# Kernel optimization log

Measured on AMD Instinct MI355X. Metric: run time of the kernel, lower is better.

Reference implementation:

```python
import jax, jax.numpy as jnp
import numpy as np

D_IN, D_H1, D_H2, D_OUT = 24, 64, 128, 64

def setup_inputs() -> dict:
    key = jax.random.key(0)
    ks = jax.random.split(key, 7)
    B, L = 256, 2048
    input_data = jax.random.normal(ks[0], (B, L, D_IN), dtype=jnp.float32)
    s = lambda fan_in: 1.0 / np.sqrt(fan_in)
    W1 = jax.random.uniform(ks[1], (D_IN, D_H1), minval=-s(D_IN), maxval=s(D_IN), dtype=jnp.float32)
    b1 = jax.random.uniform(ks[2], (D_H1,), minval=-s(D_IN), maxval=s(D_IN), dtype=jnp.float32)
    W2 = jax.random.uniform(ks[3], (D_H1, D_H2), minval=-s(D_H1), maxval=s(D_H1), dtype=jnp.float32)
    b2 = jax.random.uniform(ks[4], (D_H2,), minval=-s(D_H1), maxval=s(D_H1), dtype=jnp.float32)
    W3 = jax.random.uniform(ks[5], (D_H2, D_OUT), minval=-s(D_H2), maxval=s(D_H2), dtype=jnp.float32)
    b3 = jax.random.uniform(ks[6], (D_OUT,), minval=-s(D_H2), maxval=s(D_H2), dtype=jnp.float32)
    return {"input_data": input_data, "W1": W1, "b1": b1, "W2": W2, "b2": b2, "W3": W3, "b3": b3, "batch_size": 256}

def reference(input_data, W1, b1, W2, b2, W3, b3, batch_size):
    # Vectorized equivalent of the per-(batch,line) MLP loop:
    # three Linear+ReLU layers applied to every [24]-dim vector.
    h = jax.nn.relu(jnp.einsum('bli,ij->blj', input_data, W1) + b1)
    h = jax.nn.relu(jnp.einsum('bli,ij->blj', h, W2) + b2)
    out = jax.nn.relu(jnp.einsum('bli,ij->blj', h, W3) + b3)  # [B, L, 64]
    return out
```

## Files before the change

kernel.cpp:

```cpp
#include <hip/hip_runtime.h>

typedef float f32x4 __attribute__((ext_vector_type(4)));
typedef short s16x8 __attribute__((ext_vector_type(8)));
typedef unsigned int u32;

#define DIN 24
#define DH1 64
#define DH2 128
#define DOUT 64
#define S1 72
#define S2 136

static __device__ __forceinline__ unsigned short f2bf(float f) {
    u32 u = __builtin_bit_cast(u32, f);
    u += 0x7FFFu + ((u >> 16) & 1u);
    return (unsigned short)(u >> 16);
}

static __device__ __forceinline__ u32 cvtpk(float lo, float hi) {
    u32 r;
    asm("v_cvt_pk_bf16_f32 %0, %1, %2" : "=v"(r) : "v"(lo), "v"(hi));
    return r;
}

__global__ __launch_bounds__(256, 2) void linenet_mfma_t(
    const float* __restrict__ in,
    const float* __restrict__ W1, const float* __restrict__ b1,
    const float* __restrict__ W2, const float* __restrict__ b2,
    const float* __restrict__ W3, const float* __restrict__ b3,
    float* __restrict__ out, int M)
{
    __shared__ __align__(16) unsigned short h1lds[4][1152];
    __shared__ __align__(16) unsigned short h2lds[4][2176];

    const int tid  = threadIdx.x;
    const int wave = tid >> 6, lane = tid & 63;
    const int gl = lane >> 4, cl = lane & 15;

    s16x8 w1tf[4];
    #pragma unroll
    for (int nt = 0; nt < 4; ++nt)
        #pragma unroll
        for (int j = 0; j < 8; ++j) {
            const int k = 8 * gl + j;
            unsigned short v = 0;
            if (k < DIN)       v = f2bf(W1[k * DH1 + nt * 16 + cl]);
            else if (k == DIN) v = f2bf(b1[nt * 16 + cl]);
            w1tf[nt][j] = (short)v;
        }
    s16x8 w2tf[8][2];
    #pragma unroll
    for (int mt = 0; mt < 8; ++mt)
        #pragma unroll
        for (int ks = 0; ks < 2; ++ks)
            #pragma unroll
            for (int j = 0; j < 8; ++j)
                w2tf[mt][ks][j] =
                    (short)f2bf(W2[(32 * ks + 8 * gl + j) * DH2 + mt * 16 + cl]);
    s16x8 w3tf[4][4];
    #pragma unroll
    for (int nt = 0; nt < 4; ++nt)
        #pragma unroll
        for (int ks = 0; ks < 4; ++ks)
            #pragma unroll
            for (int j = 0; j < 8; ++j)
                w3tf[nt][ks][j] =
                    (short)f2bf(W3[(32 * ks + 8 * gl + j) * DOUT + nt * 16 + cl]);

    f32x4 b2v4[8], b3v4[4];
    #pragma unroll
    for (int mt = 0; mt < 8; ++mt) b2v4[mt] = *(const f32x4*)&b2[16 * mt + 4 * gl];
    #pragma unroll
    for (int nt = 0; nt < 4; ++nt) b3v4[nt] = *(const f32x4*)&b3[16 * nt + 4 * gl];

    unsigned short* const h1p = &h1lds[wave][0];
    unsigned short* const h2p = &h2lds[wave][0];

    const int NT = M / 16;
    const int nw = (int)gridDim.x * 4;
    int t = (int)blockIdx.x * 4 + wave;
    if (t >= NT) return;

    const int goff = (gl < 3) ? 8 * gl : 0;
    const int loff = cl * DIN + goff;

    f32x4 pf0, pf1;
    {
        const float* p = in + (size_t)t * (16 * DIN) + loff;
        pf0 = *(const f32x4*)p;
        pf1 = *(const f32x4*)(p + 4);
    }

    const f32x4 zac = {0.f, 0.f, 0.f, 0.f};

    while (t < NT) {
        u32 a1w[4];
        a1w[0] = cvtpk(pf0[0], pf0[1]);
        a1w[1] = cvtpk(pf0[2], pf0[3]);
        a1w[2] = cvtpk(pf1[0], pf1[1]);
        a1w[3] = cvtpk(pf1[2], pf1[3]);
        if (gl == 3) a1w[0] = 0x00003F80u;
        s16x8 a1;
        #pragma unroll
        for (int p = 0; p < 4; ++p) {
            a1[2 * p]     = (short)(a1w[p] & 0xFFFFu);
            a1[2 * p + 1] = (short)(a1w[p] >> 16);
        }

        const int tn = t + nw;
        {
            const int tc = (tn < NT) ? tn : t;
            const float* p = in + (size_t)tc * (16 * DIN) + loff;
            pf0 = *(const f32x4*)p;
            pf1 = *(const f32x4*)(p + 4);
        }

        f32x4 acc1[4];
        #pragma unroll
        for (int nt = 0; nt < 4; ++nt)
            acc1[nt] = __builtin_amdgcn_mfma_f32_16x16x32_bf16(w1tf[nt], a1, zac, 0, 0, 0);

        #pragma unroll
        for (int nt = 0; nt < 4; ++nt) {
            const float v0 = fmaxf(acc1[nt][0], 0.f), v1 = fmaxf(acc1[nt][1], 0.f);
            const float v2 = fmaxf(acc1[nt][2], 0.f), v3 = fmaxf(acc1[nt][3], 0.f);
            u32* w = (u32*)&h1p[cl * S1 + 16 * nt + 4 * gl];
            w[0] = cvtpk(v0, v1);
            w[1] = cvtpk(v2, v3);
        }

        s16x8 bh1[2];
        bh1[0] = *(const s16x8*)&h1p[cl * S1 + 0  + 8 * gl];
        bh1[1] = *(const s16x8*)&h1p[cl * S1 + 32 + 8 * gl];
        f32x4 acc2[8];
        #pragma unroll
        for (int mt = 0; mt < 8; ++mt)
            acc2[mt] = __builtin_amdgcn_mfma_f32_16x16x32_bf16(w2tf[mt][0], bh1[0], zac, 0, 0, 0);
        #pragma unroll
        for (int mt = 0; mt < 8; ++mt)
            acc2[mt] = __builtin_amdgcn_mfma_f32_16x16x32_bf16(w2tf[mt][1], bh1[1], acc2[mt], 0, 0, 0);

        #pragma unroll
        for (int mt = 0; mt < 8; ++mt) {
            const f32x4 s = acc2[mt] + b2v4[mt];
            const float v0 = fmaxf(s[0], 0.f), v1 = fmaxf(s[1], 0.f);
            const float v2 = fmaxf(s[2], 0.f), v3 = fmaxf(s[3], 0.f);
            u32* w = (u32*)&h2p[cl * S2 + 16 * mt + 4 * gl];
            w[0] = cvtpk(v0, v1);
            w[1] = cvtpk(v2, v3);
        }

        f32x4 acc3[4];
        #pragma unroll
        for (int ks = 0; ks < 4; ++ks) {
            const s16x8 bh2 = *(const s16x8*)&h2p[cl * S2 + 32 * ks + 8 * gl];
            #pragma unroll
            for (int nt = 0; nt < 4; ++nt)
                acc3[nt] = __builtin_amdgcn_mfma_f32_16x16x32_bf16(
                    w3tf[nt][ks], bh2, (ks == 0) ? zac : acc3[nt], 0, 0, 0);
        }

        float* const ob = out + (size_t)t * (16 * DOUT) + (size_t)cl * DOUT;
        #pragma unroll
        for (int nt = 0; nt < 4; ++nt) {
            const f32x4 s = acc3[nt] + b3v4[nt];
            f32x4 v;
            v[0] = fmaxf(s[0], 0.f); v[1] = fmaxf(s[1], 0.f);
            v[2] = fmaxf(s[2], 0.f); v[3] = fmaxf(s[3], 0.f);
            *(f32x4*)&ob[16 * nt + 4 * gl] = v;
        }

        t = tn;
    }
}

extern "C" void kernel_launch(void* const* d_in, const int* in_sizes, int n_in,
                              void* d_out, int out_size, void* d_ws, size_t ws_size,
                              hipStream_t stream)
{
    const float* in = (const float*)d_in[0];
    const float* W1 = (const float*)d_in[1];
    const float* b1 = (const float*)d_in[2];
    const float* W2 = (const float*)d_in[3];
    const float* b2 = (const float*)d_in[4];
    const float* W3 = (const float*)d_in[5];
    const float* b3 = (const float*)d_in[6];
    float* out = (float*)d_out;
    const int M = in_sizes[0] / DIN;

    dim3 grid(512), block(256);
    hipLaunchKernelGGL(linenet_mfma_t, grid, block, 0, stream,
                       in, W1, b1, W2, b2, W3, b3, out, M);
}
```

Baseline: 43.85 us.

## Move W1/W3 fragments to LDS, fold biases into accumulators, raise occupancy

W1 and W3 MFMA fragments move from per-thread registers into shared LDS, loaded once per block, to free VGPRs. Launch bounds go from 2 to 3 blocks per CU and the grid from 512 to 768. Biases b2/b3 are stored packed as bf16 and used as the initial MFMA accumulator instead of added afterwards. Layer 2 is split into halves to shorten live ranges, and outputs use nontemporal stores. The cost is extra LDS reads per tile, and biases are now rounded to bf16.

```diff
diff --git a/kernel.cpp b/kernel.cpp
--- a/kernel.cpp
+++ b/kernel.cpp
@@ -3,6 +3,8 @@
 typedef float f32x4 __attribute__((ext_vector_type(4)));
 typedef short s16x8 __attribute__((ext_vector_type(8)));
 typedef unsigned int u32;
+typedef unsigned int u32x4 __attribute__((ext_vector_type(4)));
+typedef unsigned short u16;
 
 #define DIN 24
 #define DH1 64
@@ -11,10 +13,10 @@
 #define S1 72
 #define S2 136
 
-static __device__ __forceinline__ unsigned short f2bf(float f) {
+static __device__ __forceinline__ u16 f2bf(float f) {
     u32 u = __builtin_bit_cast(u32, f);
     u += 0x7FFFu + ((u >> 16) & 1u);
-    return (unsigned short)(u >> 16);
+    return (u16)(u >> 16);
 }
 
 static __device__ __forceinline__ u32 cvtpk(float lo, float hi) {
@@ -23,31 +25,53 @@
     return r;
 }
 
-__global__ __launch_bounds__(256, 2) void linenet_mfma_t(
+static __device__ __forceinline__ float bflo(u32 pk) {
+    return __builtin_bit_cast(float, pk << 16);
+}
+static __device__ __forceinline__ float bfhi(u32 pk) {
+    return __builtin_bit_cast(float, pk & 0xFFFF0000u);
+}
+
+__global__ __launch_bounds__(256, 3) void linenet_mfma3(
     const float* __restrict__ in,
     const float* __restrict__ W1, const float* __restrict__ b1,
     const float* __restrict__ W2, const float* __restrict__ b2,
     const float* __restrict__ W3, const float* __restrict__ b3,
     float* __restrict__ out, int M)
 {
-    __shared__ __align__(16) unsigned short h1lds[4][1152];
-    __shared__ __align__(16) unsigned short h2lds[4][2176];
+    __shared__ __align__(16) u16 w1lds[4 * 64 * 8];
+    __shared__ __align__(16) u16 w3lds[16 * 64 * 8];
+    __shared__ __align__(16) u16 h1lds[4][16 * S1];
+    __shared__ __align__(16) u16 h2lds[4][16 * S2];
 
     const int tid  = threadIdx.x;
     const int wave = tid >> 6, lane = tid & 63;
     const int gl = lane >> 4, cl = lane & 15;
 
-    s16x8 w1tf[4];
-    #pragma unroll
-    for (int nt = 0; nt < 4; ++nt)
+    {
+        const int nt = tid >> 6, ln = tid & 63;
+        const int g = ln >> 4, c = ln & 15;
+        s16x8 v;
         #pragma unroll
         for (int j = 0; j < 8; ++j) {
-            const int k = 8 * gl + j;
-            unsigned short v = 0;
-            if (k < DIN)       v = f2bf(W1[k * DH1 + nt * 16 + cl]);
-            else if (k == DIN) v = f2bf(b1[nt * 16 + cl]);
-            w1tf[nt][j] = (short)v;
-        }
+            const int k = 8 * g + j;
+            u16 x = 0;
+            if (k < DIN)       x = f2bf(W1[k * DH1 + nt * 16 + c]);
+            else if (k == DIN) x = f2bf(b1[nt * 16 + c]);
+            v[j] = (short)x;
+        }
+        *(s16x8*)&w1lds[tid * 8] = v;
+    }
+    for (int it = tid; it < 16 * 64; it += 256) {
+        const int f = it >> 6, ln = it & 63;
+        const int ks = f >> 2, nt = f & 3, g = ln >> 4, c = ln & 15;
+        s16x8 v;
+        #pragma unroll
+        for (int j = 0; j < 8; ++j)
+            v[j] = (short)f2bf(W3[(32 * ks + 8 * g + j) * DOUT + nt * 16 + c]);
+        *(s16x8*)&w3lds[it * 8] = v;
+    }
+
     s16x8 w2tf[8][2];
     #pragma unroll
     for (int mt = 0; mt < 8; ++mt)
@@ -57,24 +81,25 @@
             for (int j = 0; j < 8; ++j)
                 w2tf[mt][ks][j] =
                     (short)f2bf(W2[(32 * ks + 8 * gl + j) * DH2 + mt * 16 + cl]);
-    s16x8 w3tf[4][4];
+
+    u32 b2pk[8][2], b3pk[4][2];
+    #pragma unroll
+    for (int mt = 0; mt < 8; ++mt)
+        #pragma unroll
+        for (int p = 0; p < 2; ++p)
+            b2pk[mt][p] = (u32)f2bf(b2[16 * mt + 4 * gl + 2 * p]) |
+                          ((u32)f2bf(b2[16 * mt + 4 * gl + 2 * p + 1]) << 16);
     #pragma unroll
     for (int nt = 0; nt < 4; ++nt)
         #pragma unroll
-        for (int ks = 0; ks < 4; ++ks)
-            #pragma unroll
-            for (int j = 0; j < 8; ++j)
-                w3tf[nt][ks][j] =
-                    (short)f2bf(W3[(32 * ks + 8 * gl + j) * DOUT + nt * 16 + cl]);
-
-    f32x4 b2v4[8], b3v4[4];
-    #pragma unroll
-    for (int mt = 0; mt < 8; ++mt) b2v4[mt] = *(const f32x4*)&b2[16 * mt + 4 * gl];
-    #pragma unroll
-    for (int nt = 0; nt < 4; ++nt) b3v4[nt] = *(const f32x4*)&b3[16 * nt + 4 * gl];
-
-    unsigned short* const h1p = &h1lds[wave][0];
-    unsigned short* const h2p = &h2lds[wave][0];
+        for (int p = 0; p < 2; ++p)
+            b3pk[nt][p] = (u32)f2bf(b3[16 * nt + 4 * gl + 2 * p]) |
+                          ((u32)f2bf(b3[16 * nt + 4 * gl + 2 * p + 1]) << 16);
+
+    __syncthreads();
+
+    u16* const h1p = &h1lds[wave][0];
+    u16* const h2p = &h2lds[wave][0];
 
     const int NT = M / 16;
     const int nw = (int)gridDim.x * 4;
@@ -94,18 +119,13 @@
     const f32x4 zac = {0.f, 0.f, 0.f, 0.f};
 
     while (t < NT) {
-        u32 a1w[4];
-        a1w[0] = cvtpk(pf0[0], pf0[1]);
-        a1w[1] = cvtpk(pf0[2], pf0[3]);
-        a1w[2] = cvtpk(pf1[0], pf1[1]);
-        a1w[3] = cvtpk(pf1[2], pf1[3]);
-        if (gl == 3) a1w[0] = 0x00003F80u;
-        s16x8 a1;
-        #pragma unroll
-        for (int p = 0; p < 4; ++p) {
-            a1[2 * p]     = (short)(a1w[p] & 0xFFFFu);
-            a1[2 * p + 1] = (short)(a1w[p] >> 16);
-        }
+        u32x4 aw;
+        aw[0] = cvtpk(pf0[0], pf0[1]);
+        aw[1] = cvtpk(pf0[2], pf0[3]);
+        aw[2] = cvtpk(pf1[0], pf1[1]);
+        aw[3] = cvtpk(pf1[2], pf1[3]);
+        if (gl == 3) aw[0] = 0x00003F80u;
+        const s16x8 a1 = __builtin_bit_cast(s16x8, aw);
 
         const int tn = t + nw;
         {
@@ -117,9 +137,10 @@
 
         f32x4 acc1[4];
         #pragma unroll
-        for (int nt = 0; nt < 4; ++nt)
-            acc1[nt] = __builtin_amdgcn_mfma_f32_16x16x32_bf16(w1tf[nt], a1, zac, 0, 0, 0);
-
+        for (int nt = 0; nt < 4; ++nt) {
+            const s16x8 w1f = *(const s16x8*)&w1lds[(nt * 64 + lane) * 8];
+            acc1[nt] = __builtin_amdgcn_mfma_f32_16x16x32_bf16(w1f, a1, zac, 0, 0, 0);
+        }
         #pragma unroll
         for (int nt = 0; nt < 4; ++nt) {
             const float v0 = fmaxf(acc1[nt][0], 0.f), v1 = fmaxf(acc1[nt][1], 0.f);
@@ -132,42 +153,60 @@
         s16x8 bh1[2];
         bh1[0] = *(const s16x8*)&h1p[cl * S1 + 0  + 8 * gl];
         bh1[1] = *(const s16x8*)&h1p[cl * S1 + 32 + 8 * gl];
-        f32x4 acc2[8];
-        #pragma unroll
-        for (int mt = 0; mt < 8; ++mt)
-            acc2[mt] = __builtin_amdgcn_mfma_f32_16x16x32_bf16(w2tf[mt][0], bh1[0], zac, 0, 0, 0);
-        #pragma unroll
-        for (int mt = 0; mt < 8; ++mt)
-            acc2[mt] = __builtin_amdgcn_mfma_f32_16x16x32_bf16(w2tf[mt][1], bh1[1], acc2[mt], 0, 0, 0);
-
-        #pragma unroll
-        for (int mt = 0; mt < 8; ++mt) {
-            const f32x4 s = acc2[mt] + b2v4[mt];
-            const float v0 = fmaxf(s[0], 0.f), v1 = fmaxf(s[1], 0.f);
-            const float v2 = fmaxf(s[2], 0.f), v3 = fmaxf(s[3], 0.f);
-            u32* w = (u32*)&h2p[cl * S2 + 16 * mt + 4 * gl];
-            w[0] = cvtpk(v0, v1);
-            w[1] = cvtpk(v2, v3);
+
+        #pragma unroll
+        for (int half = 0; half < 2; ++half) {
+            f32x4 acc2[4];
+            #pragma unroll
+            for (int i = 0; i < 4; ++i) {
+                const int mt = 4 * half + i;
+                f32x4 c2;
+                c2[0] = bflo(b2pk[mt][0]); c2[1] = bfhi(b2pk[mt][0]);
+                c2[2] = bflo(b2pk[mt][1]); c2[3] = bfhi(b2pk[mt][1]);
+                acc2[i] = __builtin_amdgcn_mfma_f32_16x16x32_bf16(
+                    w2tf[mt][0], bh1[0], c2, 0, 0, 0);
+            }
+            #pragma unroll
+            for (int i = 0; i < 4; ++i) {
+                const int mt = 4 * half + i;
+                acc2[i] = __builtin_amdgcn_mfma_f32_16x16x32_bf16(
+                    w2tf[mt][1], bh1[1], acc2[i], 0, 0, 0);
+            }
+            #pragma unroll
+            for (int i = 0; i < 4; ++i) {
+                const int mt = 4 * half + i;
+                const float v0 = fmaxf(acc2[i][0], 0.f), v1 = fmaxf(acc2[i][1], 0.f);
+                const float v2 = fmaxf(acc2[i][2], 0.f), v3 = fmaxf(acc2[i][3], 0.f);
+                u32* w = (u32*)&h2p[cl * S2 + 16 * mt + 4 * gl];
+                w[0] = cvtpk(v0, v1);
+                w[1] = cvtpk(v2, v3);
+            }
         }
 
         f32x4 acc3[4];
+        #pragma unroll
+        for (int nt = 0; nt < 4; ++nt) {
+            acc3[nt][0] = bflo(b3pk[nt][0]); acc3[nt][1] = bfhi(b3pk[nt][0]);
+            acc3[nt][2] = bflo(b3pk[nt][1]); acc3[nt][3] = bfhi(b3pk[nt][1]);
+        }
         #pragma unroll
         for (int ks = 0; ks < 4; ++ks) {
             const s16x8 bh2 = *(const s16x8*)&h2p[cl * S2 + 32 * ks + 8 * gl];
             #pragma unroll
-            for (int nt = 0; nt < 4; ++nt)
+            for (int nt = 0; nt < 4; ++nt) {
+                const s16x8 wf = *(const s16x8*)&w3lds[((ks * 4 + nt) * 64 + lane) * 8];
                 acc3[nt] = __builtin_amdgcn_mfma_f32_16x16x32_bf16(
-                    w3tf[nt][ks], bh2, (ks == 0) ? zac : acc3[nt], 0, 0, 0);
+                    wf, bh2, acc3[nt], 0, 0, 0);
+            }
         }
 
         float* const ob = out + (size_t)t * (16 * DOUT) + (size_t)cl * DOUT;
         #pragma unroll
         for (int nt = 0; nt < 4; ++nt) {
-            const f32x4 s = acc3[nt] + b3v4[nt];
             f32x4 v;
-            v[0] = fmaxf(s[0], 0.f); v[1] = fmaxf(s[1], 0.f);
-            v[2] = fmaxf(s[2], 0.f); v[3] = fmaxf(s[3], 0.f);
-            *(f32x4*)&ob[16 * nt + 4 * gl] = v;
+            v[0] = fmaxf(acc3[nt][0], 0.f); v[1] = fmaxf(acc3[nt][1], 0.f);
+            v[2] = fmaxf(acc3[nt][2], 0.f); v[3] = fmaxf(acc3[nt][3], 0.f);
+            __builtin_nontemporal_store(v, (f32x4*)&ob[16 * nt + 4 * gl]);
         }
 
         t = tn;
@@ -188,7 +227,7 @@
     float* out = (float*)d_out;
     const int M = in_sizes[0] / DIN;
 
-    dim3 grid(512), block(256);
-    hipLaunchKernelGGL(linenet_mfma_t, grid, block, 0, stream,
+    dim3 grid(768), block(256);
+    hipLaunchKernelGGL(linenet_mfma3, grid, block, 0, stream,
                        in, W1, b1, W2, b2, W3, b3, out, M);
 }
```

After: 52.40 us. 19.5% more time.
